# Kernel optimization log

Measured on AMD Instinct MI355X. Metric: run time of the kernel, lower is better.

The kernel has to match this reference:

```python
import jax, jax.numpy as jnp
import numpy as np

B, N, D, W, IMG = 16384, 20, 64, 64, 2048
NUM_USERS, NUM_ITEMS, NUM_INGRE = 100000, 201000, 33001


def setup_inputs() -> dict:
    key = jax.random.key(0)
    ks = jax.random.split(key, 24)
    s = lambda *sh: 1.0 / np.sqrt(sh[0])
    inp = {
        'user_input': jax.random.randint(ks[0], (B,), 0, NUM_USERS),
        'item_input': jax.random.randint(ks[1], (B,), 0, NUM_ITEMS),
        'ingre_input': jax.random.randint(ks[2], (B, N), 0, NUM_INGRE),
        'image_input': jax.random.normal(ks[3], (B, IMG), dtype=jnp.float32),
        'ingre_num': jax.random.randint(ks[4], (B,), 1, N + 1),
        'user_emb': jax.random.normal(ks[5], (NUM_USERS, D), dtype=jnp.float32) * 0.01,
        'item_emb': jax.random.normal(ks[6], (NUM_ITEMS, D), dtype=jnp.float32) * 0.01,
        'ingre_emb': jax.random.normal(ks[7], (NUM_INGRE, D), dtype=jnp.float32) * 0.01,
        'W_image_w': jax.random.normal(ks[8], (IMG, D), dtype=jnp.float32) * s(IMG),
        'W_image_b': jnp.zeros((D,), jnp.float32),
        'b_image': jnp.zeros((1, D), jnp.float32),
        'W_concat_w': jax.random.normal(ks[9], (3 * D, D), dtype=jnp.float32) * s(3 * D),
        'W_concat_b': jnp.zeros((D,), jnp.float32),
        'b_concat': jnp.zeros((1, D), jnp.float32),
        'h_w': jax.random.normal(ks[10], (D, 1), dtype=jnp.float32) * s(D),
        'h_b': jnp.zeros((1,), jnp.float32),
        'W_att_ingre_w': jax.random.normal(ks[11], (3 * D, W), dtype=jnp.float32) * s(3 * D),
        'W_att_ingre_b': jnp.zeros((W,), jnp.float32),
        'b_att_ingre': jnp.zeros((1, W), jnp.float32),
        'v': jnp.ones((W, 1), jnp.float32),
        'W_att_com_w': jax.random.normal(ks[12], (2 * D, W), dtype=jnp.float32) * s(2 * D),
        'W_att_com_b': jnp.zeros((W,), jnp.float32),
        'b_att_com': jnp.zeros((1, W), jnp.float32),
        'v_c': jnp.ones((W, 1), jnp.float32),
    }
    return inp


def reference(user_input, item_input, ingre_input, image_input, ingre_num,
              user_emb, item_emb, ingre_emb,
              W_image_w, W_image_b, b_image,
              W_concat_w, W_concat_b, b_concat, h_w, h_b,
              W_att_ingre_w, W_att_ingre_b, b_att_ingre, v,
              W_att_com_w, W_att_com_b, b_att_com, v_c):
    b = user_input.shape[0]
    ue = user_emb[user_input]                       # [B, D]
    ie = item_emb[item_input]                       # [B, D]
    qe = ingre_emb[ingre_input]                     # [B, N, D]
    img = image_input @ W_image_w + W_image_b + b_image  # [B, D]

    # ---- ingredient-level attention ----
    n = qe.shape[1]
    tile_p = jnp.broadcast_to(ue[:, None, :], (b, n, ue.shape[-1]))
    tile_i = jnp.broadcast_to(img[:, None, :], (b, n, img.shape[-1]))
    concat_v = jnp.concatenate([qe, tile_p, tile_i], axis=2)     # [B, N, 3D]
    mlp = jnp.tanh(concat_v @ W_att_ingre_w + W_att_ingre_b + b_att_ingre[0])  # [B, N, W]
    A_ = (mlp @ v)[..., 0]                                        # [B, N]
    mask = (jnp.arange(n)[None, :] < ingre_num[:, None]).astype(A_.dtype)
    A_ = A_ * mask + (1.0 - mask) * (-1e12)
    A = jax.nn.softmax(A_, axis=1)[..., None]                     # [B, N, 1]
    ingre_att = jnp.sum(A * qe, axis=1)                           # [B, D]

    # ---- component-level attention (faithful to original cat+view order) ----
    cp = jnp.concatenate([
        jnp.concatenate([ue, ie], axis=1),
        jnp.concatenate([ue, ingre_att], axis=1),
        jnp.concatenate([ue, img], axis=1),
    ], axis=0)                                                    # [3B, 2D]
    ch = jnp.tanh(cp @ W_att_com_w + W_att_com_b + b_att_com[0])  # [3B, W]
    scores = (ch @ v_c).reshape(b, -1)                            # [B, 3] (row-major, as torch .view)
    Bw = jax.nn.softmax(scores, axis=1)[..., None]                # [B, 3, 1]
    ce = jnp.stack([ie, ingre_att, img], axis=1)                  # [B, 3, D]
    item_att = jnp.sum(Bw * ce, axis=1)                           # [B, D]

    # ---- prediction head ----
    uic = jnp.concatenate([ue, item_att, ue * item_att], axis=-1) # [B, 3D]
    hidden = jax.nn.relu(uic @ W_concat_w + W_concat_b + b_concat[0])
    out = hidden @ h_w + h_b                                      # [B, 1]
    return out
```

## Files before the change

kernel.cpp:

```cpp
#include <hip/hip_runtime.h>
#include <hip/hip_fp16.h>

#define BB 16384
#define NN 20
#define DD 64
#define IMGK 2048

using bf16x8 = __attribute__((ext_vector_type(8))) short;
using f32x4  = __attribute__((ext_vector_type(4))) float;

typedef __attribute__((address_space(1))) const unsigned int GUint;
typedef __attribute__((address_space(3))) unsigned int LUint;
__device__ __forceinline__ void gl_lds16(const void* g, void* l) {
  __builtin_amdgcn_global_load_lds((GUint*)g, (LUint*)l, 16, 0, 0);
}

__device__ __forceinline__ float waveReduceSum(float x) {
#pragma unroll
  for (int off = 32; off > 0; off >>= 1) x += __shfl_xor(x, off, 64);
  return x;
}

__device__ __forceinline__ float fast_tanh(float x) {
  float e = __expf(2.f * x);
  return 1.f - __fdividef(2.f, e + 1.f);
}

__device__ __forceinline__ short f2bf(float f) {
  union { float f; unsigned u; } c; c.f = f;
  unsigned r = c.u + 0x7fffu + ((c.u >> 16) & 1u);
  return (short)(r >> 16);
}
__device__ __forceinline__ float bf2f(short s) {
  union { unsigned u; float f; } c; c.u = ((unsigned)(unsigned short)s) << 16;
  return c.f;
}
__device__ __forceinline__ short f2bf_t(float f) {
  return (short)(__float_as_uint(f) >> 16);
}

__device__ __forceinline__ unsigned pack_hi(float a, float b) {
  unsigned ua = __float_as_uint(a), ub = __float_as_uint(b);
  return (ub & 0xffff0000u) | (ua >> 16);
}
__device__ __forceinline__ float trunc_bf(float a) {
  return __uint_as_float(__float_as_uint(a) & 0xffff0000u);
}

__global__ __launch_bounds__(256)
void prep_kernel(const float* __restrict__ Wimg, const float* __restrict__ W1,
                 const float* __restrict__ Wc,
                 short* __restrict__ Wf, short* __restrict__ W1f,
                 short* __restrict__ Wcf) {
  int i = blockIdx.x * 256 + threadIdx.x;
  if (i < 32768) {
    const int lane = i & 63;
    const int h = (i >> 6) & 1;
    const int tt = (i >> 7) & 3;
    const int ks = (i >> 9) & 1;
    const int kq = i >> 10;
    const int n = 16 * tt + (lane & 15);
    const int kb = kq * 64 + ks * 32 + (lane >> 4) * 8;
    union { short s[8]; bf16x8 v; } o;
#pragma unroll
    for (int j = 0; j < 8; ++j) {
      float f = Wimg[(size_t)(kb + j) * 64 + n];
      short hi = f2bf(f);
      o.s[j] = h == 0 ? hi : f2bf(f - bf2f(hi));
    }
    reinterpret_cast<bf16x8*>(Wf)[i] = o.v;
  } else if (i < 32768 + 1536) {
    const int j = i - 32768;
    const int lane = j & 63;
    const int wt = (j >> 6) & 3;
    const int ks = j >> 8;
    const int n = 16 * wt + (lane & 15);
    const int kb = ks * 32 + (lane >> 4) * 8;
    union { short s[8]; bf16x8 v; } o;
#pragma unroll
    for (int jj = 0; jj < 8; ++jj)
      o.s[jj] = f2bf(W1[(size_t)(kb + jj) * 64 + n]);
    reinterpret_cast<bf16x8*>(W1f)[j] = o.v;
  } else if (i < 32768 + 1536 + 1024) {
    const int j = i - 32768 - 1536;
    const int lane = j & 63;
    const int wt = (j >> 6) & 3;
    const int ks = j >> 8;
    const int n = 16 * wt + (lane & 15);
    const int kb = ks * 32 + (lane >> 4) * 8;
    union { short s[8]; bf16x8 v; } o;
#pragma unroll
    for (int jj = 0; jj < 8; ++jj)
      o.s[jj] = f2bf(Wc[(size_t)(kb + jj) * 64 + n]);
    reinterpret_cast<bf16x8*>(Wcf)[j] = o.v;
  }
}

__global__ __launch_bounds__(256, 5)
void img_gemm_mfma(const float* __restrict__ img_in,
                   const short* __restrict__ Wf,
                   __half* __restrict__ pp) {
  __shared__ short wlds[8192];
  __shared__ float alds[4096];
  const int t = threadIdx.x;
  const int wave = t >> 6, lane = t & 63;
  const int lr = lane & 15, lk = lane >> 4;
  const int kq = blockIdx.x & 31, rgb = blockIdx.x >> 5;
  const int r0 = rgb * 64;
  __half* pout = pp + (size_t)kq * BB * 64;

  const short* wsrc = Wf + (size_t)kq * 8192;
#pragma unroll
  for (int i = 0; i < 4; ++i) {
    int j = i * 256 + t;
    gl_lds16(wsrc + j * 8, wlds + j * 8);
  }
#pragma unroll
  for (int i = 0; i < 4; ++i) {
    int j = i * 256 + t;
    int r = j >> 4, c = j & 15;
    int gc = (c ^ (r & 7)) * 4;
    gl_lds16(img_in + (size_t)(r0 + r) * IMGK + kq * 64 + gc, alds + j * 4);
  }
  asm volatile("s_waitcnt vmcnt(0)" ::: "memory");
  __syncthreads();

  const int arow = wave * 16 + lr;
  const int rx = arow & 7;
  float4 Af[2][2];
#pragma unroll
  for (int ks = 0; ks < 2; ++ks) {
    const int s0 = ks * 8 + lk * 2;
    Af[ks][0] = *reinterpret_cast<const float4*>(alds + arow * 64 + (s0 ^ rx) * 4);
    Af[ks][1] = *reinterpret_cast<const float4*>(alds + arow * 64 + ((s0 + 1) ^ rx) * 4);
  }
  const bf16x8* wp = reinterpret_cast<const bf16x8*>(wlds);
  f32x4 aHH[4], aER[4];
#pragma unroll
  for (int tt = 0; tt < 4; ++tt) {
    aHH[tt] = (f32x4){0.f, 0.f, 0.f, 0.f};
    aER[tt] = (f32x4){0.f, 0.f, 0.f, 0.f};
  }
#pragma unroll
  for (int ks = 0; ks < 2; ++ks) {
    float4 va = Af[ks][0], vb = Af[ks][1];
    union { unsigned u[4]; bf16x8 v; } hi, lo;
    hi.u[0] = pack_hi(va.x, va.y);
    hi.u[1] = pack_hi(va.z, va.w);
    hi.u[2] = pack_hi(vb.x, vb.y);
    hi.u[3] = pack_hi(vb.z, vb.w);
    lo.u[0] = pack_hi(va.x - trunc_bf(va.x), va.y - trunc_bf(va.y));
    lo.u[1] = pack_hi(va.z - trunc_bf(va.z), va.w - trunc_bf(va.w));
    lo.u[2] = pack_hi(vb.x - trunc_bf(vb.x), vb.y - trunc_bf(vb.y));
    lo.u[3] = pack_hi(vb.z - trunc_bf(vb.z), vb.w - trunc_bf(vb.w));
#pragma unroll
    for (int tt = 0; tt < 4; ++tt) {
      bf16x8 wh = wp[((ks * 4 + tt) * 2 + 0) * 64 + lane];
      bf16x8 wl = wp[((ks * 4 + tt) * 2 + 1) * 64 + lane];
      aHH[tt] = __builtin_amdgcn_mfma_f32_16x16x32_bf16(hi.v, wh, aHH[tt], 0, 0, 0);
      aER[tt] = __builtin_amdgcn_mfma_f32_16x16x32_bf16(hi.v, wl, aER[tt], 0, 0, 0);
      aER[tt] = __builtin_amdgcn_mfma_f32_16x16x32_bf16(lo.v, wh, aER[tt], 0, 0, 0);
    }
  }
#pragma unroll
  for (int tt = 0; tt < 4; ++tt)
#pragma unroll
    for (int r = 0; r < 4; ++r)
      alds[(size_t)(wave * 16 + 4 * lk + r) * 64 + 16 * tt + lr] = aHH[tt][r] + aER[tt][r];
  asm volatile("s_waitcnt lgkmcnt(0)" ::: "memory");
  {
    const int row_l = lane >> 2, colq = (lane & 3) * 16;
    const float* src = alds + (size_t)(wave * 16 + row_l) * 64 + colq;
    union { __half h[8]; int4 v; } o1, o2;
#pragma unroll
    for (int j = 0; j < 8; ++j) {
      o1.h[j] = __float2half(src[j]);
      o2.h[j] = __float2half(src[8 + j]);
    }
    __half* dst = pout + (size_t)(r0 + wave * 16 + row_l) * 64 + colq;
    *reinterpret_cast<int4*>(dst) = o1.v;
    *reinterpret_cast<int4*>(dst + 8) = o2.v;
  }
}

__global__ __launch_bounds__(512, 3)
void mid_kernel(const int* __restrict__ user_input,
                const int* __restrict__ item_input,
                const int* __restrict__ ingre_input,
                const int* __restrict__ ingre_num,
                const float* __restrict__ user_emb,
                const float* __restrict__ item_emb,
                const float* __restrict__ ingre_emb,
                const __half* __restrict__ pp,
                const float* __restrict__ Wb, const float* __restrict__ bimg,
                const short* __restrict__ W1f,
                const float* __restrict__ Wib, const float* __restrict__ bai,
                const float* __restrict__ v,
                const short* __restrict__ Wcf,
                const float* __restrict__ Wcb, const float* __restrict__ bac,
                const float* __restrict__ vc,
                float* __restrict__ ws_img,
                float* __restrict__ ws_ia,
                float* __restrict__ ws_flat) {
  __shared__ short wflds[12288];
  __shared__ short qe_s[8][20][72];
  __shared__ short ui_s[8][256];
  __shared__ float sc_s[8][32];
  const int t = threadIdx.x;
  const int wave = t >> 6, lane = t & 63;
  const int lr = lane & 15, lk = lane >> 4;
  const int b = blockIdx.x * 8 + wave;

  for (int i = t; i < 1536; i += 512)
    reinterpret_cast<bf16x8*>(wflds)[i] = reinterpret_cast<const bf16x8*>(W1f)[i];

  float qv[NN];
#pragma unroll
  for (int n = 0; n < NN; ++n) {
    const int gi = ingre_input[b * NN + n];
    qv[n] = ingre_emb[(size_t)gi * 64 + lane];
  }
  __half hsum = pp[(size_t)0 * BB * 64 + (size_t)b * 64 + lane];
#pragma unroll
  for (int kq = 1; kq < 32; ++kq)
    hsum = __hadd(hsum, pp[(size_t)kq * BB * 64 + (size_t)b * 64 + lane]);
  const float s = Wb[lane] + bimg[lane] + __half2float(hsum);
  const int u = user_input[b];
  const int it = item_input[b];
  const float ue = user_emb[(size_t)u * 64 + lane];
  const float iev = item_emb[(size_t)it * 64 + lane];
  ws_img[(size_t)b * 64 + lane] = s;
  float vv[4], biasw[4];
#pragma unroll
  for (int wt = 0; wt < 4; ++wt) {
    vv[wt] = v[16 * wt + lr];
    biasw[wt] = Wib[16 * wt + lr] + bai[16 * wt + lr];
  }
  const float bbc = Wcb[lane] + bac[lane];
  const float vcl = vc[lane];

#pragma unroll
  for (int n = 0; n < NN; ++n) qe_s[wave][n][lane] = f2bf_t(qv[n]);
  ui_s[wave][lane] = f2bf_t(ue);
  ui_s[wave][64 + lane] = f2bf_t(s);
  ui_s[wave][128 + lane] = f2bf_t(iev);
  __syncthreads();

  const int r1 = (16 + lr < NN) ? 16 + lr : 0;
  bf16x8 aq0[2], aq1[2], au[4];
#pragma unroll
  for (int ks = 0; ks < 2; ++ks) {
    aq0[ks] = *reinterpret_cast<const bf16x8*>(&qe_s[wave][lr][ks * 32 + lk * 8]);
    aq1[ks] = *reinterpret_cast<const bf16x8*>(&qe_s[wave][r1][ks * 32 + lk * 8]);
  }
#pragma unroll
  for (int ks = 0; ks < 4; ++ks)
    au[ks] = *reinterpret_cast<const bf16x8*>(&ui_s[wave][ks * 32 + lk * 8]);

  const bf16x8* wp = reinterpret_cast<const bf16x8*>(wflds);
  f32x4 accq[2][4], accb[4];
#pragma unroll
  for (int wt = 0; wt < 4; ++wt) {
    accq[0][wt] = (f32x4){0.f, 0.f, 0.f, 0.f};
    accq[1][wt] = (f32x4){0.f, 0.f, 0.f, 0.f};
    accb[wt] = (f32x4){0.f, 0.f, 0.f, 0.f};
  }
#pragma unroll
  for (int ks = 0; ks < 2; ++ks)
#pragma unroll
    for (int wt = 0; wt < 4; ++wt) {
      bf16x8 w = wp[(ks * 4 + wt) * 64 + lane];
      accq[0][wt] = __builtin_amdgcn_mfma_f32_16x16x32_bf16(aq0[ks], w, accq[0][wt], 0, 0, 0);
      accq[1][wt] = __builtin_amdgcn_mfma_f32_16x16x32_bf16(aq1[ks], w, accq[1][wt], 0, 0, 0);
    }
#pragma unroll
  for (int ks = 2; ks < 6; ++ks)
#pragma unroll
    for (int wt = 0; wt < 4; ++wt) {
      bf16x8 w = wp[(ks * 4 + wt) * 64 + lane];
      accb[wt] = __builtin_amdgcn_mfma_f32_16x16x32_bf16(au[ks - 2], w, accb[wt], 0, 0, 0);
    }
  float basew[4];
#pragma unroll
  for (int wt = 0; wt < 4; ++wt) basew[wt] = accb[wt][0] + biasw[wt];

  float sp[2][4];
#pragma unroll
  for (int nt = 0; nt < 2; ++nt)
#pragma unroll
    for (int r = 0; r < 4; ++r) {
      float sv = 0.f;
#pragma unroll
      for (int wt = 0; wt < 4; ++wt) {
        float x = accq[nt][wt][r] + basew[wt];
        sv = fmaf(fast_tanh(x), vv[wt], sv);
      }
      sp[nt][r] = sv;
    }
#pragma unroll
  for (int off = 1; off < 16; off <<= 1)
#pragma unroll
    for (int nt = 0; nt < 2; ++nt)
#pragma unroll
      for (int r = 0; r < 4; ++r) sp[nt][r] += __shfl_xor(sp[nt][r], off, 64);
  if (lr == 0) {
#pragma unroll
    for (int r = 0; r < 4; ++r) {
      sc_s[wave][4 * lk + r] = sp[0][r];
      sc_s[wave][16 + 4 * lk + r] = sp[1][r];
    }
  }
  asm volatile("s_waitcnt lgkmcnt(0)" ::: "memory");
  float scn[NN];
#pragma unroll
  for (int q = 0; q < 5; ++q) {
    float4 s4 = *reinterpret_cast<const float4*>(&sc_s[wave][4 * q]);
    scn[4 * q + 0] = s4.x; scn[4 * q + 1] = s4.y;
    scn[4 * q + 2] = s4.z; scn[4 * q + 3] = s4.w;
  }
  asm volatile("s_waitcnt lgkmcnt(0)" ::: "memory");
  const int num = ingre_num[b];
#pragma unroll
  for (int n = 0; n < NN; ++n) scn[n] = (n < num) ? scn[n] : -1e12f;
  float m01 = fmaxf(fmaxf(scn[0], scn[1]), scn[2]);
  float m02 = fmaxf(fmaxf(scn[3], scn[4]), scn[5]);
  float m03 = fmaxf(fmaxf(scn[6], scn[7]), scn[8]);
  float m04 = fmaxf(fmaxf(scn[9], scn[10]), scn[11]);
  float m05 = fmaxf(fmaxf(scn[12], scn[13]), scn[14]);
  float m06 = fmaxf(fmaxf(scn[15], scn[16]), scn[17]);
  float m07 = fmaxf(scn[18], scn[19]);
  float m = fmaxf(fmaxf(fmaxf(m01, m02), fmaxf(m03, m04)),
                  fmaxf(fmaxf(m05, m06), m07));
  float ssum = 0.f;
#pragma unroll
  for (int n = 0; n < NN; ++n) {
    scn[n] = __expf(scn[n] - m);
    ssum += scn[n];
  }
  const float inv = __fdividef(1.f, ssum);
  float ia = 0.f;
#pragma unroll
  for (int n = 0; n < NN; ++n) ia = fmaf(scn[n], qv[n], ia);
  ia *= inv;
  ws_ia[(size_t)b * 64 + lane] = ia;

  float* P4w = reinterpret_cast<float*>(&qe_s[wave][0][0]);
  ui_s[wave][192 + lane] = f2bf_t(ia);
  asm volatile("s_waitcnt lgkmcnt(0)" ::: "memory");
  const bf16x8 zerov = (bf16x8){0, 0, 0, 0, 0, 0, 0, 0};
  f32x4 accU[4], accY[4];
#pragma unroll
  for (int wt = 0; wt < 4; ++wt) {
    accU[wt] = (f32x4){0.f, 0.f, 0.f, 0.f};
    accY[wt] = (f32x4){0.f, 0.f, 0.f, 0.f};
  }
  const int yoff = (lr == 0) ? 128 : (lr == 1) ? 192 : 64;
#pragma unroll
  for (int ks = 0; ks < 2; ++ks) {
    bf16x8 aU = (lr == 0)
        ? *reinterpret_cast<const bf16x8*>(&ui_s[wave][ks * 32 + lk * 8]) : zerov;
    bf16x8 aY = (lr < 3)
        ? *reinterpret_cast<const bf16x8*>(&ui_s[wave][yoff + ks * 32 + lk * 8]) : zerov;
#pragma unroll
    for (int wt = 0; wt < 4; ++wt) {
      bf16x8 wU = *reinterpret_cast<const bf16x8*>(Wcf + ((ks * 4 + wt) * 64 + lane) * 8);
      bf16x8 wY = *reinterpret_cast<const bf16x8*>(Wcf + (((ks + 2) * 4 + wt) * 64 + lane) * 8);
      accU[wt] = __builtin_amdgcn_mfma_f32_16x16x32_bf16(aU, wU, accU[wt], 0, 0, 0);
      accY[wt] = __builtin_amdgcn_mfma_f32_16x16x32_bf16(aY, wY, accY[wt], 0, 0, 0);
    }
  }
  if (lk == 0) {
#pragma unroll
    for (int wt = 0; wt < 4; ++wt) {
      P4w[0 * 64 + wt * 16 + lr] = accU[wt][0];
      P4w[1 * 64 + wt * 16 + lr] = accY[wt][0];
      P4w[2 * 64 + wt * 16 + lr] = accY[wt][1];
      P4w[3 * 64 + wt * 16 + lr] = accY[wt][2];
    }
  }
  asm volatile("s_waitcnt lgkmcnt(0)" ::: "memory");
  const float su = P4w[lane] + bbc;
  float sc3[3];
#pragma unroll
  for (int c = 0; c < 3; ++c) {
    float x = su + P4w[(1 + c) * 64 + lane];
    sc3[c] = waveReduceSum(fast_tanh(x) * vcl);
  }
  if (lane == 0) {
    ws_flat[b] = sc3[0];
    ws_flat[BB + b] = sc3[1];
    ws_flat[2 * BB + b] = sc3[2];
  }
}

__global__ __launch_bounds__(256, 3)
void head_kernel(const int* __restrict__ user_input,
                 const int* __restrict__ item_input,
                 const float* __restrict__ user_emb,
                 const float* __restrict__ item_emb,
                 const float* __restrict__ Wcat,
                 const float* __restrict__ Wcatb,
                 const float* __restrict__ bcat,
                 const float* __restrict__ hw,
                 const float* __restrict__ hb,
                 const float* __restrict__ ws_img,
                 const float* __restrict__ ws_ia,
                 const float* __restrict__ ws_flat,
                 float* __restrict__ out) {
  __shared__ float Wlds[192 * 64];
  __shared__ float ue_s[4][64];
  __shared__ float itt_s[4][64];
  const int t = threadIdx.x;
  for (int i = t; i < 192 * 64 / 4; i += 256)
    reinterpret_cast<float4*>(Wlds)[i] = reinterpret_cast<const float4*>(Wcat)[i];
  __syncthreads();
  const int wave = t >> 6, lane = t & 63;
  const float bb = Wcatb[lane] + bcat[lane];
  const float hwl = hw[lane];
  const float hbv = hb[0];
  const int b0 = blockIdx.x * 16 + wave * 4;
#pragma unroll 1
  for (int bi = 0; bi < 4; ++bi) {
    const int b = b0 + bi;
    const float s0 = ws_flat[3 * b + 0];
    const float s1 = ws_flat[3 * b + 1];
    const float s2 = ws_flat[3 * b + 2];
    const float m = fmaxf(s0, fmaxf(s1, s2));
    const float e0 = __expf(s0 - m), e1 = __expf(s1 - m), e2 = __expf(s2 - m);
    const float inv = 1.0f / (e0 + e1 + e2);
    const int u = user_input[b];
    const int it = item_input[b];
    const float uev = user_emb[(size_t)u * 64 + lane];
    const float itt = (e0 * item_emb[(size_t)it * 64 + lane] +
                       e1 * ws_ia[(size_t)b * 64 + lane] +
                       e2 * ws_img[(size_t)b * 64 + lane]) * inv;
    ue_s[wave][lane] = uev;
    itt_s[wave][lane] = itt;
    asm volatile("s_waitcnt lgkmcnt(0)" ::: "memory");
    const float4* u4 = reinterpret_cast<const float4*>(&ue_s[wave][0]);
    const float4* i4 = reinterpret_cast<const float4*>(&itt_s[wave][0]);
    float h = bb;
#pragma unroll
    for (int d0 = 0; d0 < 16; ++d0) {
      float4 uu = u4[d0];
      float4 ii = i4[d0];
      int d = d0 * 4;
      h = fmaf(uu.x, Wlds[(d + 0) * 64 + lane], h);
      h = fmaf(ii.x, Wlds[(64 + d + 0) * 64 + lane], h);
      h = fmaf(uu.x * ii.x, Wlds[(128 + d + 0) * 64 + lane], h);
      h = fmaf(uu.y, Wlds[(d + 1) * 64 + lane], h);
      h = fmaf(ii.y, Wlds[(64 + d + 1) * 64 + lane], h);
      h = fmaf(uu.y * ii.y, Wlds[(128 + d + 1) * 64 + lane], h);
      h = fmaf(uu.z, Wlds[(d + 2) * 64 + lane], h);
      h = fmaf(ii.z, Wlds[(64 + d + 2) * 64 + lane], h);
      h = fmaf(uu.z * ii.z, Wlds[(128 + d + 2) * 64 + lane], h);
      h = fmaf(uu.w, Wlds[(d + 3) * 64 + lane], h);
      h = fmaf(ii.w, Wlds[(64 + d + 3) * 64 + lane], h);
      h = fmaf(uu.w * ii.w, Wlds[(128 + d + 3) * 64 + lane], h);
    }
    h = fmaxf(h, 0.f) * hwl;
    float o = waveReduceSum(h);
    if (lane == 0) out[b] = o + hbv;
    asm volatile("s_waitcnt lgkmcnt(0)" ::: "memory");
  }
}

extern "C" void kernel_launch(void* const* d_in, const int* in_sizes, int n_in,
                              void* d_out, int out_size, void* d_ws, size_t ws_size,
                              hipStream_t stream) {
  (void)in_sizes; (void)n_in; (void)out_size; (void)ws_size;
  const int* user_input = (const int*)d_in[0];
  const int* item_input = (const int*)d_in[1];
  const int* ingre_input = (const int*)d_in[2];
  const float* image_input = (const float*)d_in[3];
  const int* ingre_num = (const int*)d_in[4];
  const float* user_emb = (const float*)d_in[5];
  const float* item_emb = (const float*)d_in[6];
  const float* ingre_emb = (const float*)d_in[7];
  const float* W_image_w = (const float*)d_in[8];
  const float* W_image_b = (const float*)d_in[9];
  const float* b_image = (const float*)d_in[10];
  const float* W_concat_w = (const float*)d_in[11];
  const float* W_concat_b = (const float*)d_in[12];
  const float* b_concat = (const float*)d_in[13];
  const float* h_w = (const float*)d_in[14];
  const float* h_b = (const float*)d_in[15];
  const float* W_att_ingre_w = (const float*)d_in[16];
  const float* W_att_ingre_b = (const float*)d_in[17];
  const float* b_att_ingre = (const float*)d_in[18];
  const float* v = (const float*)d_in[19];
  const float* W_att_com_w = (const float*)d_in[20];
  const float* W_att_com_b = (const float*)d_in[21];
  const float* b_att_com = (const float*)d_in[22];
  const float* v_c = (const float*)d_in[23];

  float* ws = (float*)d_ws;
  float* ws_img = ws;
  float* ws_ia = ws + (size_t)BB * 64;
  float* ws_flat = ws + (size_t)2 * BB * 64;
  short* Wf = (short*)(ws + (size_t)2 * BB * 64 + 3 * BB);
  short* W1f = Wf + (size_t)32 * 8192;
  short* Wcf = W1f + 12288;
  __half* pp = (__half*)(Wcf + 8192);
  float* out = (float*)d_out;

  prep_kernel<<<(32768 + 1536 + 1024 + 255) / 256, 256, 0, stream>>>(
      W_image_w, W_att_ingre_w, W_att_com_w, Wf, W1f, Wcf);
  img_gemm_mfma<<<8192, 256, 0, stream>>>(image_input, Wf, pp);
  mid_kernel<<<BB / 8, 512, 0, stream>>>(user_input, item_input, ingre_input, ingre_num,
                                         user_emb, item_emb, ingre_emb, pp,
                                         W_image_b, b_image, W1f,
                                         W_att_ingre_b, b_att_ingre, v,
                                         Wcf, W_att_com_b, b_att_com, v_c,
                                         ws_img, ws_ia, ws_flat);
  head_kernel<<<BB / 16, 256, 0, stream>>>(user_input, item_input, user_emb, item_emb,
                                           W_concat_w, W_concat_b, b_concat, h_w, h_b,
                                           ws_img, ws_ia, ws_flat, out);
}
```

Before: 124.5 us.

## Process two batch rows per wave in mid_kernel with 256-thread blocks

New measurement: 153.2 us. 23.1% more time.

```diff
diff --git a/kernel.cpp b/kernel.cpp
--- a/kernel.cpp
+++ b/kernel.cpp
@@ -183,7 +183,7 @@
   }
 }
 
-__global__ __launch_bounds__(512, 3)
+__global__ __launch_bounds__(256, 3)
 void mid_kernel(const int* __restrict__ user_input,
                 const int* __restrict__ item_input,
                 const int* __restrict__ ingre_input,
@@ -209,27 +209,40 @@
   const int t = threadIdx.x;
   const int wave = t >> 6, lane = t & 63;
   const int lr = lane & 15, lk = lane >> 4;
-  const int b = blockIdx.x * 8 + wave;
-
-  for (int i = t; i < 1536; i += 512)
+  const int b0 = blockIdx.x * 8 + wave * 2;
+
+  for (int i = t; i < 1536; i += 256)
     reinterpret_cast<bf16x8*>(wflds)[i] = reinterpret_cast<const bf16x8*>(W1f)[i];
 
-  float qv[NN];
-#pragma unroll
-  for (int n = 0; n < NN; ++n) {
-    const int gi = ingre_input[b * NN + n];
-    qv[n] = ingre_emb[(size_t)gi * 64 + lane];
-  }
-  __half hsum = pp[(size_t)0 * BB * 64 + (size_t)b * 64 + lane];
+  float qv[2][NN];
+#pragma unroll
+  for (int n = 0; n < NN; ++n)
+#pragma unroll
+    for (int p = 0; p < 2; ++p) {
+      const int gi = ingre_input[(b0 + p) * NN + n];
+      qv[p][n] = ingre_emb[(size_t)gi * 64 + lane];
+    }
+  __half hs[2];
+#pragma unroll
+  for (int p = 0; p < 2; ++p)
+    hs[p] = pp[(size_t)(b0 + p) * 64 + lane];
 #pragma unroll
   for (int kq = 1; kq < 32; ++kq)
-    hsum = __hadd(hsum, pp[(size_t)kq * BB * 64 + (size_t)b * 64 + lane]);
-  const float s = Wb[lane] + bimg[lane] + __half2float(hsum);
-  const int u = user_input[b];
-  const int it = item_input[b];
-  const float ue = user_emb[(size_t)u * 64 + lane];
-  const float iev = item_emb[(size_t)it * 64 + lane];
-  ws_img[(size_t)b * 64 + lane] = s;
+#pragma unroll
+    for (int p = 0; p < 2; ++p)
+      hs[p] = __hadd(hs[p], pp[(size_t)kq * BB * 64 + (size_t)(b0 + p) * 64 + lane]);
+  float sImg[2], ueV[2], ieV[2];
+  int numN[2];
+#pragma unroll
+  for (int p = 0; p < 2; ++p) {
+    sImg[p] = Wb[lane] + bimg[lane] + __half2float(hs[p]);
+    const int u = user_input[b0 + p];
+    const int it = item_input[b0 + p];
+    ueV[p] = user_emb[(size_t)u * 64 + lane];
+    ieV[p] = item_emb[(size_t)it * 64 + lane];
+    numN[p] = ingre_num[b0 + p];
+    ws_img[(size_t)(b0 + p) * 64 + lane] = sImg[p];
+  }
   float vv[4], biasw[4];
 #pragma unroll
   for (int wt = 0; wt < 4; ++wt) {
@@ -240,156 +253,191 @@
   const float vcl = vc[lane];
 
 #pragma unroll
-  for (int n = 0; n < NN; ++n) qe_s[wave][n][lane] = f2bf_t(qv[n]);
-  ui_s[wave][lane] = f2bf_t(ue);
-  ui_s[wave][64 + lane] = f2bf_t(s);
-  ui_s[wave][128 + lane] = f2bf_t(iev);
+  for (int p = 0; p < 2; ++p) {
+    const int sl = wave * 2 + p;
+#pragma unroll
+    for (int n = 0; n < NN; ++n) qe_s[sl][n][lane] = f2bf_t(qv[p][n]);
+    ui_s[sl][lane] = f2bf_t(ueV[p]);
+    ui_s[sl][64 + lane] = f2bf_t(sImg[p]);
+    ui_s[sl][128 + lane] = f2bf_t(ieV[p]);
+  }
   __syncthreads();
 
   const int r1 = (16 + lr < NN) ? 16 + lr : 0;
-  bf16x8 aq0[2], aq1[2], au[4];
-#pragma unroll
-  for (int ks = 0; ks < 2; ++ks) {
-    aq0[ks] = *reinterpret_cast<const bf16x8*>(&qe_s[wave][lr][ks * 32 + lk * 8]);
-    aq1[ks] = *reinterpret_cast<const bf16x8*>(&qe_s[wave][r1][ks * 32 + lk * 8]);
-  }
-#pragma unroll
-  for (int ks = 0; ks < 4; ++ks)
-    au[ks] = *reinterpret_cast<const bf16x8*>(&ui_s[wave][ks * 32 + lk * 8]);
-
+  bf16x8 aq0[2][2], aq1[2][2], au[2][4];
+#pragma unroll
+  for (int p = 0; p < 2; ++p) {
+    const int sl = wave * 2 + p;
+#pragma unroll
+    for (int ks = 0; ks < 2; ++ks) {
+      aq0[p][ks] = *reinterpret_cast<const bf16x8*>(&qe_s[sl][lr][ks * 32 + lk * 8]);
+      aq1[p][ks] = *reinterpret_cast<const bf16x8*>(&qe_s[sl][r1][ks * 32 + lk * 8]);
+    }
+#pragma unroll
+    for (int ks = 0; ks < 4; ++ks)
+      au[p][ks] = *reinterpret_cast<const bf16x8*>(&ui_s[sl][ks * 32 + lk * 8]);
+  }
   const bf16x8* wp = reinterpret_cast<const bf16x8*>(wflds);
-  f32x4 accq[2][4], accb[4];
-#pragma unroll
-  for (int wt = 0; wt < 4; ++wt) {
-    accq[0][wt] = (f32x4){0.f, 0.f, 0.f, 0.f};
-    accq[1][wt] = (f32x4){0.f, 0.f, 0.f, 0.f};
-    accb[wt] = (f32x4){0.f, 0.f, 0.f, 0.f};
-  }
+  f32x4 accq[2][2][4], accb[2][4];
+#pragma unroll
+  for (int p = 0; p < 2; ++p)
+#pragma unroll
+    for (int wt = 0; wt < 4; ++wt) {
+      accq[p][0][wt] = (f32x4){0.f, 0.f, 0.f, 0.f};
+      accq[p][1][wt] = (f32x4){0.f, 0.f, 0.f, 0.f};
+      accb[p][wt] = (f32x4){0.f, 0.f, 0.f, 0.f};
+    }
 #pragma unroll
   for (int ks = 0; ks < 2; ++ks)
 #pragma unroll
     for (int wt = 0; wt < 4; ++wt) {
       bf16x8 w = wp[(ks * 4 + wt) * 64 + lane];
-      accq[0][wt] = __builtin_amdgcn_mfma_f32_16x16x32_bf16(aq0[ks], w, accq[0][wt], 0, 0, 0);
-      accq[1][wt] = __builtin_amdgcn_mfma_f32_16x16x32_bf16(aq1[ks], w, accq[1][wt], 0, 0, 0);
+#pragma unroll
+      for (int p = 0; p < 2; ++p) {
+        accq[p][0][wt] = __builtin_amdgcn_mfma_f32_16x16x32_bf16(aq0[p][ks], w, accq[p][0][wt], 0, 0, 0);
+        accq[p][1][wt] = __builtin_amdgcn_mfma_f32_16x16x32_bf16(aq1[p][ks], w, accq[p][1][wt], 0, 0, 0);
+      }
     }
 #pragma unroll
   for (int ks = 2; ks < 6; ++ks)
 #pragma unroll
     for (int wt = 0; wt < 4; ++wt) {
       bf16x8 w = wp[(ks * 4 + wt) * 64 + lane];
-      accb[wt] = __builtin_amdgcn_mfma_f32_16x16x32_bf16(au[ks - 2], w, accb[wt], 0, 0, 0);
-    }
-  float basew[4];
-#pragma unroll
-  for (int wt = 0; wt < 4; ++wt) basew[wt] = accb[wt][0] + biasw[wt];
-
-  float sp[2][4];
-#pragma unroll
-  for (int nt = 0; nt < 2; ++nt)
-#pragma unroll
-    for (int r = 0; r < 4; ++r) {
-      float sv = 0.f;
-#pragma unroll
-      for (int wt = 0; wt < 4; ++wt) {
-        float x = accq[nt][wt][r] + basew[wt];
-        sv = fmaf(fast_tanh(x), vv[wt], sv);
+#pragma unroll
+      for (int p = 0; p < 2; ++p)
+        accb[p][wt] = __builtin_amdgcn_mfma_f32_16x16x32_bf16(au[p][ks - 2], w, accb[p][wt], 0, 0, 0);
+    }
+  float sp[2][2][4];
+#pragma unroll
+  for (int p = 0; p < 2; ++p)
+#pragma unroll
+    for (int nt = 0; nt < 2; ++nt)
+#pragma unroll
+      for (int r = 0; r < 4; ++r) {
+        float sv = 0.f;
+#pragma unroll
+        for (int wt = 0; wt < 4; ++wt) {
+          float x = accq[p][nt][wt][r] + accb[p][wt][0] + biasw[wt];
+          sv = fmaf(fast_tanh(x), vv[wt], sv);
+        }
+        sp[p][nt][r] = sv;
       }
-      sp[nt][r] = sv;
-    }
 #pragma unroll
   for (int off = 1; off < 16; off <<= 1)
 #pragma unroll
-    for (int nt = 0; nt < 2; ++nt)
-#pragma unroll
-      for (int r = 0; r < 4; ++r) sp[nt][r] += __shfl_xor(sp[nt][r], off, 64);
+    for (int p = 0; p < 2; ++p)
+#pragma unroll
+      for (int nt = 0; nt < 2; ++nt)
+#pragma unroll
+        for (int r = 0; r < 4; ++r) sp[p][nt][r] += __shfl_xor(sp[p][nt][r], off, 64);
   if (lr == 0) {
 #pragma unroll
-    for (int r = 0; r < 4; ++r) {
-      sc_s[wave][4 * lk + r] = sp[0][r];
-      sc_s[wave][16 + 4 * lk + r] = sp[1][r];
-    }
+    for (int p = 0; p < 2; ++p)
+#pragma unroll
+      for (int r = 0; r < 4; ++r) {
+        sc_s[wave * 2 + p][4 * lk + r] = sp[p][0][r];
+        sc_s[wave * 2 + p][16 + 4 * lk + r] = sp[p][1][r];
+      }
   }
   asm volatile("s_waitcnt lgkmcnt(0)" ::: "memory");
-  float scn[NN];
-#pragma unroll
-  for (int q = 0; q < 5; ++q) {
-    float4 s4 = *reinterpret_cast<const float4*>(&sc_s[wave][4 * q]);
-    scn[4 * q + 0] = s4.x; scn[4 * q + 1] = s4.y;
-    scn[4 * q + 2] = s4.z; scn[4 * q + 3] = s4.w;
+
+  float iaV[2];
+#pragma unroll
+  for (int p = 0; p < 2; ++p) {
+    const int sl = wave * 2 + p;
+    float scn[NN];
+#pragma unroll
+    for (int q = 0; q < 5; ++q) {
+      float4 s4 = *reinterpret_cast<const float4*>(&sc_s[sl][4 * q]);
+      scn[4 * q + 0] = s4.x; scn[4 * q + 1] = s4.y;
+      scn[4 * q + 2] = s4.z; scn[4 * q + 3] = s4.w;
+    }
+    asm volatile("s_waitcnt lgkmcnt(0)" ::: "memory");
+#pragma unroll
+    for (int n = 0; n < NN; ++n) scn[n] = (n < numN[p]) ? scn[n] : -1e12f;
+    float m01 = fmaxf(fmaxf(scn[0], scn[1]), scn[2]);
+    float m02 = fmaxf(fmaxf(scn[3], scn[4]), scn[5]);
+    float m03 = fmaxf(fmaxf(scn[6], scn[7]), scn[8]);
+    float m04 = fmaxf(fmaxf(scn[9], scn[10]), scn[11]);
+    float m05 = fmaxf(fmaxf(scn[12], scn[13]), scn[14]);
+    float m06 = fmaxf(fmaxf(scn[15], scn[16]), scn[17]);
+    float m07 = fmaxf(scn[18], scn[19]);
+    float m = fmaxf(fmaxf(fmaxf(m01, m02), fmaxf(m03, m04)),
+                    fmaxf(fmaxf(m05, m06), m07));
+    float ssum = 0.f;
+#pragma unroll
+    for (int n = 0; n < NN; ++n) {
+      scn[n] = __expf(scn[n] - m);
+      ssum += scn[n];
+    }
+    const float inv = __fdividef(1.f, ssum);
+    float ia = 0.f;
+#pragma unroll
+    for (int n = 0; n < NN; ++n) ia = fmaf(scn[n], qv[p][n], ia);
+    ia *= inv;
+    iaV[p] = ia;
+    ws_ia[(size_t)(b0 + p) * 64 + lane] = ia;
+    ui_s[sl][192 + lane] = f2bf_t(ia);
   }
   asm volatile("s_waitcnt lgkmcnt(0)" ::: "memory");
-  const int num = ingre_num[b];
-#pragma unroll
-  for (int n = 0; n < NN; ++n) scn[n] = (n < num) ? scn[n] : -1e12f;
-  float m01 = fmaxf(fmaxf(scn[0], scn[1]), scn[2]);
-  float m02 = fmaxf(fmaxf(scn[3], scn[4]), scn[5]);
-  float m03 = fmaxf(fmaxf(scn[6], scn[7]), scn[8]);
-  float m04 = fmaxf(fmaxf(scn[9], scn[10]), scn[11]);
-  float m05 = fmaxf(fmaxf(scn[12], scn[13]), scn[14]);
-  float m06 = fmaxf(fmaxf(scn[15], scn[16]), scn[17]);
-  float m07 = fmaxf(scn[18], scn[19]);
-  float m = fmaxf(fmaxf(fmaxf(m01, m02), fmaxf(m03, m04)),
-                  fmaxf(fmaxf(m05, m06), m07));
-  float ssum = 0.f;
-#pragma unroll
-  for (int n = 0; n < NN; ++n) {
-    scn[n] = __expf(scn[n] - m);
-    ssum += scn[n];
-  }
-  const float inv = __fdividef(1.f, ssum);
-  float ia = 0.f;
-#pragma unroll
-  for (int n = 0; n < NN; ++n) ia = fmaf(scn[n], qv[n], ia);
-  ia *= inv;
-  ws_ia[(size_t)b * 64 + lane] = ia;
-
-  float* P4w = reinterpret_cast<float*>(&qe_s[wave][0][0]);
-  ui_s[wave][192 + lane] = f2bf_t(ia);
-  asm volatile("s_waitcnt lgkmcnt(0)" ::: "memory");
+
   const bf16x8 zerov = (bf16x8){0, 0, 0, 0, 0, 0, 0, 0};
-  f32x4 accU[4], accY[4];
-#pragma unroll
-  for (int wt = 0; wt < 4; ++wt) {
-    accU[wt] = (f32x4){0.f, 0.f, 0.f, 0.f};
-    accY[wt] = (f32x4){0.f, 0.f, 0.f, 0.f};
-  }
+  f32x4 accU[2][4], accY[2][4];
+#pragma unroll
+  for (int p = 0; p < 2; ++p)
+#pragma unroll
+    for (int wt = 0; wt < 4; ++wt) {
+      accU[p][wt] = (f32x4){0.f, 0.f, 0.f, 0.f};
+      accY[p][wt] = (f32x4){0.f, 0.f, 0.f, 0.f};
+    }
   const int yoff = (lr == 0) ? 128 : (lr == 1) ? 192 : 64;
 #pragma unroll
   for (int ks = 0; ks < 2; ++ks) {
-    bf16x8 aU = (lr == 0)
-        ? *reinterpret_cast<const bf16x8*>(&ui_s[wave][ks * 32 + lk * 8]) : zerov;
-    bf16x8 aY = (lr < 3)
-        ? *reinterpret_cast<const bf16x8*>(&ui_s[wave][yoff + ks * 32 + lk * 8]) : zerov;
 #pragma unroll
     for (int wt = 0; wt < 4; ++wt) {
       bf16x8 wU = *reinterpret_cast<const bf16x8*>(Wcf + ((ks * 4 + wt) * 64 + lane) * 8);
       bf16x8 wY = *reinterpret_cast<const bf16x8*>(Wcf + (((ks + 2) * 4 + wt) * 64 + lane) * 8);
-      accU[wt] = __builtin_amdgcn_mfma_f32_16x16x32_bf16(aU, wU, accU[wt], 0, 0, 0);
-      accY[wt] = __builtin_amdgcn_mfma_f32_16x16x32_bf16(aY, wY, accY[wt], 0, 0, 0);
-    }
-  }
-  if (lk == 0) {
-#pragma unroll
-    for (int wt = 0; wt < 4; ++wt) {
-      P4w[0 * 64 + wt * 16 + lr] = accU[wt][0];
-      P4w[1 * 64 + wt * 16 + lr] = accY[wt][0];
-      P4w[2 * 64 + wt * 16 + lr] = accY[wt][1];
-      P4w[3 * 64 + wt * 16 + lr] = accY[wt][2];
+#pragma unroll
+      for (int p = 0; p < 2; ++p) {
+        const int sl = wave * 2 + p;
+        bf16x8 aU = (lr == 0)
+            ? *reinterpret_cast<const bf16x8*>(&ui_s[sl][ks * 32 + lk * 8]) : zerov;
+        bf16x8 aY = (lr < 3)
+            ? *reinterpret_cast<const bf16x8*>(&ui_s[sl][yoff + ks * 32 + lk * 8]) : zerov;
+        accU[p][wt] = __builtin_amdgcn_mfma_f32_16x16x32_bf16(aU, wU, accU[p][wt], 0, 0, 0);
+        accY[p][wt] = __builtin_amdgcn_mfma_f32_16x16x32_bf16(aY, wY, accY[p][wt], 0, 0, 0);
+      }
+    }
+  }
+#pragma unroll
+  for (int p = 0; p < 2; ++p) {
+    float* P4w = reinterpret_cast<float*>(&qe_s[wave * 2 + p][0][0]);
+    if (lk == 0) {
+#pragma unroll
+      for (int wt = 0; wt < 4; ++wt) {
+        P4w[0 * 64 + wt * 16 + lr] = accU[p][wt][0];
+        P4w[1 * 64 + wt * 16 + lr] = accY[p][wt][0];
+        P4w[2 * 64 + wt * 16 + lr] = accY[p][wt][1];
+        P4w[3 * 64 + wt * 16 + lr] = accY[p][wt][2];
+      }
     }
   }
   asm volatile("s_waitcnt lgkmcnt(0)" ::: "memory");
-  const float su = P4w[lane] + bbc;
-  float sc3[3];
-#pragma unroll
-  for (int c = 0; c < 3; ++c) {
-    float x = su + P4w[(1 + c) * 64 + lane];
-    sc3[c] = waveReduceSum(fast_tanh(x) * vcl);
-  }
-  if (lane == 0) {
-    ws_flat[b] = sc3[0];
-    ws_flat[BB + b] = sc3[1];
-    ws_flat[2 * BB + b] = sc3[2];
+#pragma unroll
+  for (int p = 0; p < 2; ++p) {
+    const float* P4w = reinterpret_cast<const float*>(&qe_s[wave * 2 + p][0][0]);
+    const float su = P4w[lane] + bbc;
+    float sc3[3];
+#pragma unroll
+    for (int c = 0; c < 3; ++c) {
+      float x = su + P4w[(1 + c) * 64 + lane];
+      sc3[c] = waveReduceSum(fast_tanh(x) * vcl);
+    }
+    if (lane == 0) {
+      ws_flat[b0 + p] = sc3[0];
+      ws_flat[BB + b0 + p] = sc3[1];
+      ws_flat[2 * BB + b0 + p] = sc3[2];
+    }
   }
 }
 
@@ -507,7 +555,7 @@
   prep_kernel<<<(32768 + 1536 + 1024 + 255) / 256, 256, 0, stream>>>(
       W_image_w, W_att_ingre_w, W_att_com_w, Wf, W1f, Wcf);
   img_gemm_mfma<<<8192, 256, 0, stream>>>(image_input, Wf, pp);
-  mid_kernel<<<BB / 8, 512, 0, stream>>>(user_input, item_input, ingre_input, ingre_num,
+  mid_kernel<<<BB / 8, 256, 0, stream>>>(user_input, item_input, ingre_input, ingre_num,
                                          user_emb, item_emb, ingre_emb, pp,
                                          W_image_b, b_image, W1f,
                                          W_att_ingre_b, b_att_ingre, v,
```
